# Kernel optimization log

Hardware: AMD Instinct MI355X
Metric: run time of the kernel (lower is better)

Reference implementation:

```python
import jax, jax.numpy as jnp
import numpy as np

ALPHA = 0.2  # LeakyReLU negative slope


def setup_inputs() -> dict:
    key = jax.random.key(0)
    k1, k2, k3, k4 = jax.random.split(key, 4)
    N, F_in, F_out = 8192, 512, 64
    x = jax.random.normal(k1, (N, F_in), dtype=jnp.float32)
    adj = jax.random.uniform(k2, (N, N), dtype=jnp.float32)
    W = jax.random.normal(k3, (F_in, F_out), dtype=jnp.float32) * 0.05
    a = jax.random.normal(k4, (2 * F_out, 1), dtype=jnp.float32) * 0.05
    return {"x": x, "adj": adj, "W": W, "a": a}


def reference(x, adj, W, a):
    F_out = W.shape[1]
    h = x @ W                                   # [N, F_out]
    # Additive attention decomposed: score[i,j] = h[i]·a1 + h[j]·a2
    # (equivalent to concat([h_i, h_j]) @ a, without the N×N×2F blowup)
    a1 = a[:F_out, 0]                           # [F_out]
    a2 = a[F_out:, 0]                           # [F_out]
    e = jax.nn.leaky_relu(h @ a1[:, None] + (h @ a2)[None, :], ALPHA)  # [N, N]
    attention = jax.nn.softmax(e * adj, axis=1)  # elementwise mult, as in source
    # dropout skipped (eval / training=False -> identity)
    h_prime = attention @ h                      # [N, F_out]
    return jax.nn.elu(h_prime)                   # concat=True branch
```

## Files before the change

kernel.cpp:

```cpp
#include <hip/hip_runtime.h>

#define ALPHA 0.2f

typedef __attribute__((ext_vector_type(8))) short short8v;
typedef __attribute__((ext_vector_type(4))) float f32x4;

__device__ __forceinline__ unsigned cvt_pk_bf16(float a, float b) {
  unsigned d;
  asm("v_cvt_pk_bf16_f32 %0, %1, %2" : "=v"(d) : "v"(a), "v"(b));
  return d;
}

#define GLOAD_LDS16(gp, lp)                                                   \
  __builtin_amdgcn_global_load_lds(                                           \
      (const __attribute__((address_space(1))) unsigned int*)(gp),            \
      (__attribute__((address_space(3))) unsigned int*)(lp), 16, 0, 0)

__global__ __launch_bounds__(256) void k1_proj(
    const float* __restrict__ x, const float* __restrict__ W,
    const float* __restrict__ avec,
    short* __restrict__ hT, float* __restrict__ s1, float* __restrict__ s2,
    float* __restrict__ num) {
  __shared__ float xl[32 * 132];
  __shared__ float Wl[128 * 64];
  const int t   = threadIdx.x;
  const int rb  = blockIdx.x;
  const int row = t >> 3;
  const int fg  = t & 7;

  {
    float4 z = {0.f, 0.f, 0.f, 0.f};
    *(float4*)(num + rb * 2048 + t * 8)     = z;
    *(float4*)(num + rb * 2048 + t * 8 + 4) = z;
  }

  float acc[8];
#pragma unroll
  for (int e = 0; e < 8; e++) acc[e] = 0.f;

  for (int kc = 0; kc < 4; kc++) {
#pragma unroll
    for (int u = 0; u < 4; u++) {
      int lin = t + u * 256;
      int r = lin >> 5, c4 = lin & 31;
      float4 v = *(const float4*)(x + (size_t)(rb * 32 + r) * 512 + kc * 128 + c4 * 4);
      *(float4*)(xl + r * 132 + c4 * 4) = v;
    }
#pragma unroll
    for (int u = 0; u < 8; u++) {
      int lin = t + u * 256;
      int r = lin >> 4, c4 = lin & 15;
      float4 v = *(const float4*)(W + (size_t)(kc * 128 + r) * 64 + c4 * 4);
      *(float4*)(Wl + r * 64 + c4 * 4) = v;
    }
    __syncthreads();
#pragma unroll 8
    for (int k = 0; k < 128; k++) {
      float xv = xl[row * 132 + k];
      float4 w0 = *(const float4*)(Wl + k * 64 + fg * 8);
      float4 w1 = *(const float4*)(Wl + k * 64 + fg * 8 + 4);
      acc[0] = fmaf(xv, w0.x, acc[0]); acc[1] = fmaf(xv, w0.y, acc[1]);
      acc[2] = fmaf(xv, w0.z, acc[2]); acc[3] = fmaf(xv, w0.w, acc[3]);
      acc[4] = fmaf(xv, w1.x, acc[4]); acc[5] = fmaf(xv, w1.y, acc[5]);
      acc[6] = fmaf(xv, w1.z, acc[6]); acc[7] = fmaf(xv, w1.w, acc[7]);
    }
    __syncthreads();
  }

  float p1 = 0.f, p2 = 0.f;
#pragma unroll
  for (int e = 0; e < 8; e++) {
    p1 = fmaf(acc[e], avec[fg * 8 + e], p1);
    p2 = fmaf(acc[e], avec[64 + fg * 8 + e], p2);
  }
  p1 += __shfl_xor(p1, 1, 64); p1 += __shfl_xor(p1, 2, 64); p1 += __shfl_xor(p1, 4, 64);
  p2 += __shfl_xor(p2, 1, 64); p2 += __shfl_xor(p2, 2, 64); p2 += __shfl_xor(p2, 4, 64);
  const int gi = rb * 32 + row;
  if (fg == 0) { s1[gi] = p1; s2[gi] = p2; }
#pragma unroll
  for (int e = 0; e < 8; e++) {
    union { float f; unsigned u; } v; v.f = acc[e];
    unsigned rr = v.u + 0x7fffu + ((v.u >> 16) & 1u);
    hT[(size_t)(fg * 8 + e) * 8192 + gi] = (short)(rr >> 16);
  }
}

__global__ __launch_bounds__(256, 2) void k2_attn(
    const float* __restrict__ adj, const short* __restrict__ hT,
    const float* __restrict__ s1, const float* __restrict__ s2,
    float* __restrict__ num, float* __restrict__ den) {
  __shared__ short hP[32768];
  __shared__ short Pl[8192];
  const int t    = threadIdx.x;
  const int wvi  = t >> 6;
  const int l    = t & 63;
  const int lq   = l >> 4;
  const int lr   = l & 15;
  const int rb   = blockIdx.x & 127;
  const int ks   = blockIdx.x >> 7;
  const int r0   = rb << 6;
  const int j0   = ks << 9;

  float  s1own = s1[r0 + wvi * 16 + lr];
  float4 s2A4  = *(const float4*)(s2 + j0 + l * 4);
  float4 s2B4  = *(const float4*)(s2 + j0 + 256 + l * 4);

#pragma unroll
  for (int r = 0; r < 16; r++) {
    const int d    = r * 4096 + t * 16;
    const int frow = d >> 10;
    const int lcb  = (d & 1023) ^ ((frow & 7) << 4);
    GLOAD_LDS16(hT + (size_t)frow * 8192 + j0 + (lcb >> 1), (char*)hP + d);
  }

  const float* ar = adj + (size_t)(r0 + wvi * 16) * 8192 + j0 + l * 4;
  float4 A0,A1,A2,A3,A4,A5,A6,A7,A8,A9,A10,A11,A12,A13,A14,A15;
  A0  = *(const float4*)(ar);
  A1  = *(const float4*)(ar + 1 * 8192);
  A2  = *(const float4*)(ar + 2 * 8192);
  A3  = *(const float4*)(ar + 3 * 8192);
  A4  = *(const float4*)(ar + 4 * 8192);
  A5  = *(const float4*)(ar + 5 * 8192);
  A6  = *(const float4*)(ar + 6 * 8192);
  A7  = *(const float4*)(ar + 7 * 8192);
  A8  = *(const float4*)(ar + 8 * 8192);
  A9  = *(const float4*)(ar + 9 * 8192);
  A10 = *(const float4*)(ar + 10 * 8192);
  A11 = *(const float4*)(ar + 11 * 8192);
  A12 = *(const float4*)(ar + 12 * 8192);
  A13 = *(const float4*)(ar + 13 * 8192);
  A14 = *(const float4*)(ar + 14 * 8192);
  A15 = *(const float4*)(ar + 15 * 8192);

  __syncthreads();
  __builtin_amdgcn_sched_barrier(0);

  float4 B0,B1,B2,B3,B4,B5,B6,B7,B8,B9,B10,B11,B12,B13,B14,B15;
  B0  = *(const float4*)(ar + 256);
  B1  = *(const float4*)(ar + 1 * 8192 + 256);
  B2  = *(const float4*)(ar + 2 * 8192 + 256);
  B3  = *(const float4*)(ar + 3 * 8192 + 256);
  B4  = *(const float4*)(ar + 4 * 8192 + 256);
  B5  = *(const float4*)(ar + 5 * 8192 + 256);
  B6  = *(const float4*)(ar + 6 * 8192 + 256);
  B7  = *(const float4*)(ar + 7 * 8192 + 256);
  B8  = *(const float4*)(ar + 8 * 8192 + 256);
  B9  = *(const float4*)(ar + 9 * 8192 + 256);
  B10 = *(const float4*)(ar + 10 * 8192 + 256);
  B11 = *(const float4*)(ar + 11 * 8192 + 256);
  B12 = *(const float4*)(ar + 12 * 8192 + 256);
  B13 = *(const float4*)(ar + 13 * 8192 + 256);
  B14 = *(const float4*)(ar + 14 * 8192 + 256);
  B15 = *(const float4*)(ar + 15 * 8192 + 256);

  float s1r[16];
#pragma unroll
  for (int i = 0; i < 16; i++) s1r[i] = __shfl(s1own, i, 64);

  float denom_p[16];
#pragma unroll
  for (int i = 0; i < 16; i++) denom_p[i] = 0.f;
  f32x4 acc[4];
#pragma unroll
  for (int fb = 0; fb < 4; fb++) acc[fb] = (f32x4){0.f, 0.f, 0.f, 0.f};

  char* Pw = (char*)Pl + wvi * 4096;
  unsigned pk0[16], pk1[16];

#define EXPROW4(I, AV, S2V) do {                                              \
    float z0 = s1r[I] + S2V.x; z0 = fmaxf(z0, ALPHA * z0) * AV.x;             \
    float z1 = s1r[I] + S2V.y; z1 = fmaxf(z1, ALPHA * z1) * AV.y;             \
    float z2 = s1r[I] + S2V.z; z2 = fmaxf(z2, ALPHA * z2) * AV.z;             \
    float z3 = s1r[I] + S2V.w; z3 = fmaxf(z3, ALPHA * z3) * AV.w;             \
    float w0 = __expf(z0), w1 = __expf(z1), w2 = __expf(z2), w3 = __expf(z3); \
    denom_p[I] += (w0 + w1) + (w2 + w3);                                      \
    pk0[I] = cvt_pk_bf16(w0, w1); pk1[I] = cvt_pk_bf16(w2, w3);               \
  } while (0)

#define PWRITE(HALF) do {                                                     \
    if ((l >> 5) == (HALF)) {                                                 \
      const int cb = (l & 31) * 8;                                            \
      _Pragma("unroll")                                                       \
      for (int i2 = 0; i2 < 16; i2++) {                                       \
        uint2 pv; pv.x = pk0[i2]; pv.y = pk1[i2];                             \
        *(uint2*)(Pw + (((i2 << 8) + cb) ^ ((i2 & 7) << 4))) = pv;            \
      }                                                                       \
    }                                                                         \
  } while (0)

#define MFMACHUNK(CL) do {                                                    \
    __builtin_amdgcn_s_setprio(1);                                            \
    _Pragma("unroll")                                                         \
    for (int kk = 0; kk < 4; kk++) {                                          \
      const int ab = ((lr << 8) + (kk << 6) + (lq << 4)) ^ ((lr & 7) << 4);   \
      const short8v au = *(const short8v*)(Pw + ab);                          \
      _Pragma("unroll")                                                       \
      for (int fb = 0; fb < 4; fb++) {                                        \
        const int fr = fb * 16 + lr;                                          \
        const int bb = ((fr << 10) + ((CL) << 8) + (kk << 6) + (lq << 4))     \
                       ^ ((fr & 7) << 4);                                     \
        const short8v bu = *(const short8v*)((char*)hP + bb);                 \
        acc[fb] = __builtin_amdgcn_mfma_f32_16x16x32_bf16(au, bu,             \
                                                          acc[fb], 0, 0, 0); \
      }                                                                       \
    }                                                                         \
    __builtin_amdgcn_s_setprio(0);                                            \
  } while (0)

  EXPROW4(0, A0, s2A4);   EXPROW4(1, A1, s2A4);   EXPROW4(2, A2, s2A4);
  EXPROW4(3, A3, s2A4);   EXPROW4(4, A4, s2A4);   EXPROW4(5, A5, s2A4);
  EXPROW4(6, A6, s2A4);   EXPROW4(7, A7, s2A4);   EXPROW4(8, A8, s2A4);
  EXPROW4(9, A9, s2A4);   EXPROW4(10, A10, s2A4); EXPROW4(11, A11, s2A4);
  EXPROW4(12, A12, s2A4); EXPROW4(13, A13, s2A4); EXPROW4(14, A14, s2A4);
  EXPROW4(15, A15, s2A4);
  PWRITE(0); MFMACHUNK(0);
  PWRITE(1); MFMACHUNK(1);

  EXPROW4(0, B0, s2B4);   EXPROW4(1, B1, s2B4);   EXPROW4(2, B2, s2B4);
  EXPROW4(3, B3, s2B4);   EXPROW4(4, B4, s2B4);   EXPROW4(5, B5, s2B4);
  EXPROW4(6, B6, s2B4);   EXPROW4(7, B7, s2B4);   EXPROW4(8, B8, s2B4);
  EXPROW4(9, B9, s2B4);   EXPROW4(10, B10, s2B4); EXPROW4(11, B11, s2B4);
  EXPROW4(12, B12, s2B4); EXPROW4(13, B13, s2B4); EXPROW4(14, B14, s2B4);
  EXPROW4(15, B15, s2B4);
  PWRITE(0); MFMACHUNK(2);
  PWRITE(1); MFMACHUNK(3);

#undef EXPROW4
#undef PWRITE
#undef MFMACHUNK

#pragma unroll
  for (int i = 0; i < 16; i++) {
    float d = denom_p[i];
    d += __shfl_xor(d, 1, 64); d += __shfl_xor(d, 2, 64);
    d += __shfl_xor(d, 4, 64); d += __shfl_xor(d, 8, 64);
    d += __shfl_xor(d, 16, 64); d += __shfl_xor(d, 32, 64);
    if (l == 0) den[(size_t)ks * 8192 + r0 + wvi * 16 + i] = d;
  }
#pragma unroll
  for (int fb = 0; fb < 4; fb++)
#pragma unroll
    for (int r = 0; r < 4; r++)
      atomicAdd(&num[(size_t)(r0 + wvi * 16 + lq * 4 + r) * 64 + fb * 16 + lr],
                acc[fb][r]);
}

__global__ __launch_bounds__(256) void k3_norm(
    const float* __restrict__ num, const float* __restrict__ den,
    float* __restrict__ out) {
  const int idx = blockIdx.x * 256 + threadIdx.x;
  const int row = idx >> 6;
  float d = 0.f;
#pragma unroll
  for (int ksi = 0; ksi < 16; ksi++) d += den[ksi * 8192 + row];
  float v = num[idx] / d;
  out[idx] = v > 0.f ? v : (__expf(v) - 1.f);
}

extern "C" void kernel_launch(void* const* d_in, const int* in_sizes, int n_in,
                              void* d_out, int out_size, void* d_ws, size_t ws_size,
                              hipStream_t stream) {
  const float* x   = (const float*)d_in[0];
  const float* adj = (const float*)d_in[1];
  const float* W   = (const float*)d_in[2];
  const float* av  = (const float*)d_in[3];
  float* out = (float*)d_out;
  char* ws = (char*)d_ws;

  short* hT  = (short*)ws;
  float* s1  = (float*)(ws + (1 << 20));
  float* s2  = (float*)(ws + (1 << 20) + 32768);
  float* num = (float*)(ws + (1 << 20) + 65536);
  float* den = num + 524288u;

  hipLaunchKernelGGL(k1_proj, dim3(256), dim3(256), 0, stream,
                     x, W, av, hT, s1, s2, num);
  hipLaunchKernelGGL(k2_attn, dim3(2048), dim3(256), 0, stream,
                     adj, hT, s1, s2, num, den);
  hipLaunchKernelGGL(k3_norm, dim3(2048), dim3(256), 0, stream, num, den, out);
}
```

Baseline: 90.85 us.

## Split x@W projection along K with atomic accumulation and separate finalize kernel

The projection GEMM now splits the 512-wide reduction into four chunks across blocks, with each thread computing a 4x8 register tile and reading x straight from global memory. Partial sums are combined with float atomics into a new fp32 buffer. A second small kernel then computes the attention scores and the bf16 transposed h from that buffer. num and hacc are cleared with one memset instead of inside the kernel. This adds two launches (memset and finalize) and about half a million atomics in exchange for more register reuse in the GEMM.

```diff
diff --git a/kernel.cpp b/kernel.cpp
--- a/kernel.cpp
+++ b/kernel.cpp
@@ -16,70 +16,92 @@
       (const __attribute__((address_space(1))) unsigned int*)(gp),            \
       (__attribute__((address_space(3))) unsigned int*)(lp), 16, 0, 0)
 
-__global__ __launch_bounds__(256) void k1_proj(
+__global__ __launch_bounds__(256) void k1_gemm(
     const float* __restrict__ x, const float* __restrict__ W,
-    const float* __restrict__ avec,
-    short* __restrict__ hT, float* __restrict__ s1, float* __restrict__ s2,
-    float* __restrict__ num) {
-  __shared__ float xl[32 * 132];
+    float* __restrict__ hacc) {
   __shared__ float Wl[128 * 64];
-  const int t   = threadIdx.x;
-  const int rb  = blockIdx.x;
-  const int row = t >> 3;
-  const int fg  = t & 7;
-
-  {
-    float4 z = {0.f, 0.f, 0.f, 0.f};
-    *(float4*)(num + rb * 2048 + t * 8)     = z;
-    *(float4*)(num + rb * 2048 + t * 8 + 4) = z;
-  }
-
-  float acc[8];
-#pragma unroll
-  for (int e = 0; e < 8; e++) acc[e] = 0.f;
-
-  for (int kc = 0; kc < 4; kc++) {
-#pragma unroll
-    for (int u = 0; u < 4; u++) {
-      int lin = t + u * 256;
-      int r = lin >> 5, c4 = lin & 31;
-      float4 v = *(const float4*)(x + (size_t)(rb * 32 + r) * 512 + kc * 128 + c4 * 4);
-      *(float4*)(xl + r * 132 + c4 * 4) = v;
+  const int t    = threadIdx.x;
+  const int rblk = blockIdx.x & 63;
+  const int kc   = blockIdx.x >> 6;
+  const int r0   = rblk << 7;
+  const int k0   = kc << 7;
+  const int fg   = t & 7;
+  const int rq   = t >> 3;
+
+#pragma unroll
+  for (int u = 0; u < 8; u++) {
+    int lin = t + u * 256;
+    int r = lin >> 4, c4 = lin & 15;
+    float4 v = *(const float4*)(W + (size_t)(k0 + r) * 64 + c4 * 4);
+    *(float4*)(Wl + r * 64 + c4 * 4) = v;
+  }
+  __syncthreads();
+
+  const int rr = r0 + rq * 4;
+  float acc[4][8];
+#pragma unroll
+  for (int i = 0; i < 4; i++)
+#pragma unroll
+    for (int e = 0; e < 8; e++) acc[i][e] = 0.f;
+
+  for (int ks = 0; ks < 8; ks++) {
+    float4 xr[16];
+#pragma unroll
+    for (int i = 0; i < 4; i++)
+#pragma unroll
+      for (int j = 0; j < 4; j++)
+        xr[i * 4 + j] = *(const float4*)(
+            x + (size_t)(rr + i) * 512 + k0 + ks * 16 + j * 4);
+#pragma unroll
+    for (int k = 0; k < 16; k++) {
+      float4 w0 = *(const float4*)(Wl + (ks * 16 + k) * 64 + fg * 8);
+      float4 w1 = *(const float4*)(Wl + (ks * 16 + k) * 64 + fg * 8 + 4);
+#pragma unroll
+      for (int i = 0; i < 4; i++) {
+        const float4 xv4 = xr[i * 4 + (k >> 2)];
+        const float xv = (k & 3) == 0 ? xv4.x : (k & 3) == 1 ? xv4.y
+                        : (k & 3) == 2 ? xv4.z : xv4.w;
+        acc[i][0] = fmaf(xv, w0.x, acc[i][0]);
+        acc[i][1] = fmaf(xv, w0.y, acc[i][1]);
+        acc[i][2] = fmaf(xv, w0.z, acc[i][2]);
+        acc[i][3] = fmaf(xv, w0.w, acc[i][3]);
+        acc[i][4] = fmaf(xv, w1.x, acc[i][4]);
+        acc[i][5] = fmaf(xv, w1.y, acc[i][5]);
+        acc[i][6] = fmaf(xv, w1.z, acc[i][6]);
+        acc[i][7] = fmaf(xv, w1.w, acc[i][7]);
+      }
     }
-#pragma unroll
-    for (int u = 0; u < 8; u++) {
-      int lin = t + u * 256;
-      int r = lin >> 4, c4 = lin & 15;
-      float4 v = *(const float4*)(W + (size_t)(kc * 128 + r) * 64 + c4 * 4);
-      *(float4*)(Wl + r * 64 + c4 * 4) = v;
-    }
-    __syncthreads();
-#pragma unroll 8
-    for (int k = 0; k < 128; k++) {
-      float xv = xl[row * 132 + k];
-      float4 w0 = *(const float4*)(Wl + k * 64 + fg * 8);
-      float4 w1 = *(const float4*)(Wl + k * 64 + fg * 8 + 4);
-      acc[0] = fmaf(xv, w0.x, acc[0]); acc[1] = fmaf(xv, w0.y, acc[1]);
-      acc[2] = fmaf(xv, w0.z, acc[2]); acc[3] = fmaf(xv, w0.w, acc[3]);
-      acc[4] = fmaf(xv, w1.x, acc[4]); acc[5] = fmaf(xv, w1.y, acc[5]);
-      acc[6] = fmaf(xv, w1.z, acc[6]); acc[7] = fmaf(xv, w1.w, acc[7]);
-    }
-    __syncthreads();
-  }
+  }
+
+#pragma unroll
+  for (int i = 0; i < 4; i++)
+#pragma unroll
+    for (int e = 0; e < 8; e++)
+      atomicAdd(&hacc[(size_t)(rr + i) * 64 + fg * 8 + e], acc[i][e]);
+}
+
+__global__ __launch_bounds__(256) void k1b_fin(
+    const float* __restrict__ hacc, const float* __restrict__ avec,
+    short* __restrict__ hT, float* __restrict__ s1, float* __restrict__ s2) {
+  const int t  = threadIdx.x;
+  const int gi = blockIdx.x * 32 + (t >> 3);
+  const int fg = t & 7;
+  float4 h0 = *(const float4*)(hacc + (size_t)gi * 64 + fg * 8);
+  float4 h1 = *(const float4*)(hacc + (size_t)gi * 64 + fg * 8 + 4);
+  float hv[8] = {h0.x, h0.y, h0.z, h0.w, h1.x, h1.y, h1.z, h1.w};
 
   float p1 = 0.f, p2 = 0.f;
 #pragma unroll
   for (int e = 0; e < 8; e++) {
-    p1 = fmaf(acc[e], avec[fg * 8 + e], p1);
-    p2 = fmaf(acc[e], avec[64 + fg * 8 + e], p2);
+    p1 = fmaf(hv[e], avec[fg * 8 + e], p1);
+    p2 = fmaf(hv[e], avec[64 + fg * 8 + e], p2);
   }
   p1 += __shfl_xor(p1, 1, 64); p1 += __shfl_xor(p1, 2, 64); p1 += __shfl_xor(p1, 4, 64);
   p2 += __shfl_xor(p2, 1, 64); p2 += __shfl_xor(p2, 2, 64); p2 += __shfl_xor(p2, 4, 64);
-  const int gi = rb * 32 + row;
   if (fg == 0) { s1[gi] = p1; s2[gi] = p2; }
 #pragma unroll
   for (int e = 0; e < 8; e++) {
-    union { float f; unsigned u; } v; v.f = acc[e];
+    union { float f; unsigned u; } v; v.f = hv[e];
     unsigned rr = v.u + 0x7fffu + ((v.u >> 16) & 1u);
     hT[(size_t)(fg * 8 + e) * 8192 + gi] = (short)(rr >> 16);
   }
@@ -267,14 +289,18 @@
   float* out = (float*)d_out;
   char* ws = (char*)d_ws;
 
-  short* hT  = (short*)ws;
-  float* s1  = (float*)(ws + (1 << 20));
-  float* s2  = (float*)(ws + (1 << 20) + 32768);
-  float* num = (float*)(ws + (1 << 20) + 65536);
-  float* den = num + 524288u;
-
-  hipLaunchKernelGGL(k1_proj, dim3(256), dim3(256), 0, stream,
-                     x, W, av, hT, s1, s2, num);
+  short* hT   = (short*)ws;
+  float* s1   = (float*)(ws + (1 << 20));
+  float* s2   = (float*)(ws + (1 << 20) + 32768);
+  float* num  = (float*)(ws + (1 << 20) + 65536);
+  float* hacc = num + 524288u;
+  float* den  = hacc + 524288u;
+
+  hipMemsetAsync(num, 0, 4u << 20, stream);
+
+  hipLaunchKernelGGL(k1_gemm, dim3(256), dim3(256), 0, stream, x, W, hacc);
+  hipLaunchKernelGGL(k1b_fin, dim3(256), dim3(256), 0, stream,
+                     hacc, av, hT, s1, s2);
   hipLaunchKernelGGL(k2_attn, dim3(2048), dim3(256), 0, stream,
                      adj, hT, s1, s2, num, den);
   hipLaunchKernelGGL(k3_norm, dim3(2048), dim3(256), 0, stream, num, den, out);
```

Measured after the change: 153.2 us. 1.69x slower.
